# Optimization experiments

Hardware: AMD Instinct MI355X
Metric: run time of the kernel (lower is better)

## Reference

```python
import jax, jax.numpy as jnp
import numpy as np

AGENT, WIN = 6, 7

def _rel_pos_index(d, h, w):
    # same construction as the torch buffer `relative_position_index`
    coords = np.stack(np.meshgrid(np.arange(d), np.arange(h), np.arange(w), indexing='ij'))
    cf = coords.reshape(3, -1)                                   # [3, S]
    rc = (cf[:, :, None] - cf[:, None, :]).transpose(1, 2, 0).astype(np.int64)
    rc[:, :, 0] += d - 1; rc[:, :, 1] += h - 1; rc[:, :, 2] += w - 1
    rc[:, :, 0] *= (2 * h - 1) * (2 * w - 1)
    rc[:, :, 1] *= (2 * w - 1)
    return jnp.asarray(rc.sum(-1))                               # [S, S]

def setup_inputs() -> dict:
    key = jax.random.key(0)
    ks = jax.random.split(key, 11)
    b, L, X, Y, w1, w2, dim = 2, AGENT, 8, 8, WIN, WIN, 256
    heads, ch, nt = 8, 32, 2
    table = (2 * L - 1) * (2 * w1 - 1) * (2 * w2 - 1)
    f = lambda k, s: (0.02 * jax.random.normal(k, s)).astype(jnp.float32)
    return dict(
        x=jax.random.normal(ks[0], (b, L, X, Y, w1, w2, dim), jnp.float32),
        Wq=f(ks[1], (nt, dim, dim)), bq=f(ks[2], (nt, dim)),
        Wk=f(ks[3], (nt, dim, dim)), bk=f(ks[4], (nt, dim)),
        Wv=f(ks[5], (nt, dim, dim)), bv=f(ks[6], (nt, dim)),
        rel_att=f(ks[7], (nt * nt, heads, ch, ch)),
        rel_msg=f(ks[8], (nt * nt, heads, ch, ch)),
        bias_table=f(ks[9], (table, heads)),
        Wo=f(ks[10], (dim, dim)),
        agent_type=1,
    )

def reference(x, Wq, bq, Wk, bk, Wv, bv, rel_att, rel_msg, bias_table, Wo, agent_type):
    b, L, X, Y, w1, w2, dim = x.shape
    heads, ch = rel_att.shape[1], rel_att.shape[2]
    nt = Wq.shape[0]
    scale = ch ** -0.5
    # types = [0] + (agent_size-1)*[type], identical across batch (as in forward)
    types = jnp.concatenate([jnp.zeros(1, jnp.int32),
                             jnp.full((L - 1,), agent_type, jnp.int32)])

    def proj(W, bias):
        # type-indexed per-agent linear (gathered batched matmul instead of python loops)
        y = jnp.einsum('blxyuvd,lde->blxyuve', x, W[types])
        y = y + bias[types][None, :, None, None, None, None, :]
        # -> [b, n=(X*Y) windows, m heads, L agents, p=(w1*w2) tokens, c]
        return y.reshape(b, L, X * Y, w1 * w2, heads, ch).transpose(0, 2, 4, 1, 3, 5)

    q = proj(Wq, bq) * scale
    k = proj(Wk, bk)
    v = proj(Wv, bv)

    # relation weights gathered by (src_type, dst_type) pair: [m, L, L, c, c]
    rel = types[:, None] * nt + types[None, :]
    w_att = rel_att[rel].transpose(2, 0, 1, 3, 4)
    w_msg = rel_msg[rel].transpose(2, 0, 1, 3, 4)

    # bilinear hetero attention scores, grouped by agent pair (i,j)
    sim = jnp.einsum('bnmipc,mijcf,bnmjqf->bnmipjq', q, w_att, k)
    S, n = L * w1 * w2, X * Y
    sim = sim.reshape(b, n, heads, S, S)
    idx = _rel_pos_index(L, w1, w2)                                # [S, S] static
    sim = sim + bias_table[idx].transpose(2, 0, 1)                 # + [m, S, S] rel-pos bias
    attn = jax.nn.softmax(sim, axis=-1).reshape(b, n, heads, L, w1 * w2, L, w1 * w2)

    # relation-transformed messages, then attention-weighted aggregation
    vt = jnp.einsum('mijcf,bnmjqf->bnmijqc', w_msg, v)
    out = jnp.einsum('bnmipjq,bnmijqc->bnmipc', attn, vt)
    # [b, n, m, L, p, c] -> [b, L, X, Y, w1, w2, dim]
    out = out.transpose(0, 3, 1, 4, 2, 5).reshape(b, L, X, Y, w1, w2, dim)
    return out @ Wo.T
```

## Files before the change

kernel.cpp:

```cpp
#include <hip/hip_runtime.h>
#include <hip/hip_bf16.h>

typedef __hip_bfloat16 bf16;
typedef unsigned short u16;
typedef short bf16x8 __attribute__((ext_vector_type(8)));
typedef float f32x4  __attribute__((ext_vector_type(4)));

#define BB    2
#define LL    6
#define NWIN  64
#define PP    49
#define DIMM  256
#define HEADS 8
#define CHN   32
#define SS    294
#define ASTRIDE 264
#define BSTRIDE 304
#define WBSTRIDE 168

__device__ __forceinline__ u16 bfbits(float x) { return __bfloat16_as_ushort(__float2bfloat16(x)); }
__device__ __forceinline__ f32x4 mfma16(bf16x8 a, bf16x8 b, f32x4 c) {
    return __builtin_amdgcn_mfma_f32_16x16x32_bf16(a, b, c, 0, 0, 0);
}

__global__ __launch_bounds__(256) void k_prep(
    const float* __restrict__ Wq, const float* __restrict__ Wk, const float* __restrict__ Wv,
    const float* __restrict__ Wo, const float* __restrict__ ra, const float* __restrict__ rm,
    const float* __restrict__ bt,
    u16* __restrict__ wT, u16* __restrict__ Wob, u16* __restrict__ raT, u16* __restrict__ rmb,
    float* __restrict__ biasM)
{
    const int blk = blockIdx.x;
    if (blk < 1792) {
        const int idx = blk*256 + threadIdx.x;
        if (idx >= 7*65536) return;
        const int mat = idx >> 16, rem = idx & 65535;
        if (mat < 6) {
            const int tz = mat >> 1, t = mat & 1;
            const int e = rem >> 8, d = rem & 255;
            const float* W = (tz == 0 ? Wq : tz == 1 ? Wk : Wv);
            wT[mat*65536 + rem] = bfbits(W[t*65536 + d*256 + e]);
        } else {
            Wob[rem] = bfbits(Wo[rem]);
        }
    } else if (blk < 1920) {
        const int idx = (blk - 1792)*256 + threadIdx.x;
        if (idx < 4*HEADS*CHN*CHN) {
            const int pm = idx >> 10, cf = idx & 1023, c = cf >> 5, f = cf & 31;
            raT[(pm << 10) + (f << 5) + c] = bfbits(ra[idx]);
            rmb[idx] = bfbits(rm[idx]);
        }
    } else {
        const int idx = (blk - 1920)*256 + threadIdx.x;
        if (idx < HEADS*SS*BSTRIDE) {
            const int m = idx / (SS*BSTRIDE);
            const int rem = idx % (SS*BSTRIDE);
            const int s1 = rem / BSTRIDE, s2 = rem % BSTRIDE;
            float val = 0.f;
            if (s2 < SS) {
                const int i1 = s1/49, p1 = s1 - i1*49, h1 = p1/7, w1 = p1 - h1*7;
                const int j2 = s2/49, p2 = s2 - j2*49, h2 = p2/7, w2 = p2 - h2*7;
                const int rc = i1*169 + h1*13 + w1, cc = j2*169 + h2*13 + w2;
                val = bt[(rc - cc + 929)*8 + m];
            }
            biasM[idx] = val;
        }
    }
}

__global__ __launch_bounds__(256) void k_qkv2(
    const float* __restrict__ x, const u16* __restrict__ wT,
    const float* __restrict__ bq, const float* __restrict__ bk, const float* __restrict__ bv,
    const int* __restrict__ atype,
    u16* __restrict__ q, u16* __restrict__ k, u16* __restrict__ v)
{
    __shared__ __align__(16) u16 As[64*ASTRIDE];
    const int tid = threadIdx.x;
    const int w = tid >> 6, lane = tid & 63;
    const int g4 = lane >> 4, c16 = lane & 15;
    const int bid = blockIdx.x;
    const int nwin = bid & 63;
    const int l = (bid >> 6) % LL;
    const int b = bid / (LL*NWIN);

    const float4* xp = (const float4*)(x + (size_t)bid * (PP*DIMM));
    for (int idx = tid; idx < 49*64; idx += 256) {
        const int row = idx >> 6, c4 = idx & 63;
        const float4 xv = xp[idx];
        ushort4 h;
        h.x = bfbits(xv.x); h.y = bfbits(xv.y); h.z = bfbits(xv.z); h.w = bfbits(xv.w);
        *(ushort4*)&As[row*ASTRIDE + c4*4] = h;
    }
    const ushort4 z4 = {0, 0, 0, 0};
    for (int idx = tid; idx < 15*66; idx += 256) {
        const int row = 49 + idx/66, c4 = idx%66;
        *(ushort4*)&As[row*ASTRIDE + c4*4] = z4;
    }
    __syncthreads();

    const int t = (l == 0) ? 0 : atype[0];
    const f32x4 zero4 = {0.f, 0.f, 0.f, 0.f};

    for (int tz = 0; tz < 3; ++tz) {
        const u16* WT = wT + (size_t)(tz*2 + t)*65536;
        const float* bias = (tz == 0 ? bq : tz == 1 ? bk : bv) + t*DIMM;
        u16* dst = (tz == 0 ? q : tz == 1 ? k : v);
        const float scale = (tz == 0) ? 0.17677669529663687f : 1.0f;

        f32x4 acc[4][4];
        #pragma unroll
        for (int mm = 0; mm < 4; ++mm)
            #pragma unroll
            for (int nn = 0; nn < 4; ++nn) acc[mm][nn] = zero4;

        for (int ks = 0; ks < 8; ++ks) {
            bf16x8 a[4], bb[4];
            #pragma unroll
            for (int mm = 0; mm < 4; ++mm)
                a[mm] = *(const bf16x8*)&As[(mm*16 + c16)*ASTRIDE + ks*32 + g4*8];
            #pragma unroll
            for (int nn = 0; nn < 4; ++nn)
                bb[nn] = *(const bf16x8*)&WT[(size_t)(w*64 + nn*16 + c16)*256 + ks*32 + g4*8];
            #pragma unroll
            for (int mm = 0; mm < 4; ++mm)
                #pragma unroll
                for (int nn = 0; nn < 4; ++nn)
                    acc[mm][nn] = mfma16(a[mm], bb[nn], acc[mm][nn]);
        }

        #pragma unroll
        for (int nn = 0; nn < 4; ++nn) {
            const int col = w*64 + nn*16 + c16;
            const float bval = bias[col];
            const int head = col >> 5, c = col & 31;
            const size_t base = (((size_t)(b*NWIN + nwin)*HEADS + head)*SS + l*PP)*CHN + c;
            #pragma unroll
            for (int mm = 0; mm < 4; ++mm) {
                #pragma unroll
                for (int r = 0; r < 4; ++r) {
                    const int row = mm*16 + g4*4 + r;
                    if (row < PP)
                        dst[base + (size_t)row*CHN] = bfbits((acc[mm][nn][r] + bval)*scale);
                }
            }
        }
    }
}

__global__ __launch_bounds__(256) void k_attn(
    const u16* __restrict__ q, const u16* __restrict__ kk_, const u16* __restrict__ v,
    const u16* __restrict__ raT, const u16* __restrict__ rmb,
    const float* __restrict__ biasM, const int* __restrict__ atype,
    u16* __restrict__ o_pre)
{
    __shared__ __align__(16) u16 vT[32*328];
    __shared__ __align__(16) u16 vT0[32*72];
    __shared__ __align__(16) u16 wbuf[4*16*WBSTRIDE];

    const int tid  = threadIdx.x;
    const int w    = tid >> 6;
    const int lane = tid & 63;
    const int g4   = lane >> 4;
    const int c16  = lane & 15;
    const int bid  = blockIdx.x;
    const int m    = bid & 7;
    const int nwin = (bid >> 3) & 63;
    const int b    = bid >> 9;
    const int at   = atype[0];

    const size_t slab = (size_t)bid * (SS*CHN);
    const u16* qs  = q   + slab;
    const u16* ksg = kk_ + slab;
    const u16* vsg = v   + slab;
    const float* bm = biasM + (size_t)m*(SS*BSTRIDE);

    u16* wb = wbuf + w*(16*WBSTRIDE);

    for (int idx = tid; idx < 32*26; idx += 256) vT[(idx/26)*328 + 294 + (idx%26)] = 0;
    for (int idx = tid; idx < 32*15; idx += 256) vT0[(idx/15)*72 + 49 + (idx%15)] = 0;
    for (int idx = tid; idx < SS*CHN/2; idx += 256) {
        const int s2 = idx >> 4;
        const int f2 = (idx & 15) << 1;
        const unsigned int val = *(const unsigned int*)(vsg + s2*CHN + f2);
        const u16 v0 = (u16)(val & 0xffff), v1 = (u16)(val >> 16);
        vT[f2*328 + s2] = v0;
        vT[(f2+1)*328 + s2] = v1;
        if (s2 < 49) { vT0[f2*72 + s2] = v0; vT0[(f2+1)*72 + s2] = v1; }
    }
    __syncthreads();

    const f32x4 zero4 = {0.f, 0.f, 0.f, 0.f};

    for (int job = w; job < 20; job += 4) {
        const int tile = (job == 19) ? 3 : job;
        const int tiv  = (job <= 3) ? 0 : at;
        const int pair0 = tiv*2;
        const int pair1 = tiv*2 + at;

        const int rowA = tile*16 + c16;
        const bf16x8 aq = *(const bf16x8*)(qs + rowA*CHN + g4*8);
        f32x4 cqw00, cqw01, cqw10, cqw11;
        {
            const u16* base0 = raT + (pair0*HEADS + m)*1024;
            const u16* base1 = raT + (pair1*HEADS + m)*1024;
            const bf16x8 b00 = *(const bf16x8*)(base0 + (c16     )*32 + g4*8);
            const bf16x8 b01 = *(const bf16x8*)(base0 + (16 + c16)*32 + g4*8);
            const bf16x8 b10 = *(const bf16x8*)(base1 + (c16     )*32 + g4*8);
            const bf16x8 b11 = *(const bf16x8*)(base1 + (16 + c16)*32 + g4*8);
            cqw00 = mfma16(aq, b00, zero4);
            cqw01 = mfma16(aq, b01, zero4);
            cqw10 = mfma16(aq, b10, zero4);
            cqw11 = mfma16(aq, b11, zero4);
        }
        #pragma unroll
        for (int r = 0; r < 4; ++r) {
            const int row = g4*4 + r;
            wb[row*72 +      c16] = bfbits(cqw00[r]);
            wb[row*72 + 16 + c16] = bfbits(cqw01[r]);
            wb[row*72 + 32 + c16] = bfbits(cqw10[r]);
            wb[row*72 + 48 + c16] = bfbits(cqw11[r]);
        }
        const bf16x8 A0 = *(const bf16x8*)(wb + c16*72 +      g4*8);
        const bf16x8 A1 = *(const bf16x8*)(wb + c16*72 + 32 + g4*8);

        f32x4 acc[19];
        #pragma unroll
        for (int t = 0; t < 3; ++t) {
            const bf16x8 bk = *(const bf16x8*)(ksg + (t*16 + c16)*CHN + g4*8);
            acc[t] = mfma16(A0, bk, zero4);
        }
        {
            const bf16x8 bk = *(const bf16x8*)(ksg + (3*16 + c16)*CHN + g4*8);
            const f32x4 cA = mfma16(A0, bk, zero4);
            const f32x4 cB = mfma16(A1, bk, zero4);
            #pragma unroll
            for (int r = 0; r < 4; ++r) acc[3][r] = (c16 == 0) ? cA[r] : cB[r];
        }
        #pragma unroll
        for (int t = 4; t < 19; ++t) {
            const bf16x8 bk = *(const bf16x8*)(ksg + (t*16 + c16)*CHN + g4*8);
            acc[t] = mfma16(A1, bk, zero4);
        }

        const float* bmrow[4];
        #pragma unroll
        for (int r = 0; r < 4; ++r) {
            const int s1r = tile*16 + g4*4 + r;
            const int s1c = (s1r < SS) ? s1r : 293;
            bmrow[r] = bm + (size_t)s1c*BSTRIDE;
        }
        #pragma unroll
        for (int t = 0; t < 19; ++t)
            #pragma unroll
            for (int r = 0; r < 4; ++r)
                acc[t][r] += bmrow[r][t*16 + c16];
        #pragma unroll
        for (int r = 0; r < 4; ++r)
            acc[18][r] = (c16 < 6) ? acc[18][r] : -1e30f;

        float mx[4], sm[4];
        #pragma unroll
        for (int r = 0; r < 4; ++r) mx[r] = -1e30f;
        #pragma unroll
        for (int t = 0; t < 19; ++t)
            #pragma unroll
            for (int r = 0; r < 4; ++r) mx[r] = fmaxf(mx[r], acc[t][r]);
        #pragma unroll
        for (int off = 1; off < 16; off <<= 1)
            #pragma unroll
            for (int r = 0; r < 4; ++r) mx[r] = fmaxf(mx[r], __shfl_xor(mx[r], off));
        #pragma unroll
        for (int r = 0; r < 4; ++r) sm[r] = 0.f;
        #pragma unroll
        for (int t = 0; t < 19; ++t)
            #pragma unroll
            for (int r = 0; r < 4; ++r) { const float e = __expf(acc[t][r] - mx[r]); acc[t][r] = e; sm[r] += e; }
        #pragma unroll
        for (int off = 1; off < 16; off <<= 1)
            #pragma unroll
            for (int r = 0; r < 4; ++r) sm[r] += __shfl_xor(sm[r], off);
        #pragma unroll
        for (int r = 0; r < 4; ++r) {
            const float inv = 1.0f / sm[r];
            #pragma unroll
            for (int t = 0; t < 19; ++t) acc[t][r] *= inv;
        }

        f32x4 aggF0a = zero4, aggF0b = zero4, aggF1a = zero4, aggF1b = zero4;
        f32x4 agg00 = zero4, agg01 = zero4;
        bf16x8 asave0, asave1;
        #pragma unroll
        for (int t = 0; t < 10; ++t)
            #pragma unroll
            for (int r = 0; r < 4; ++r)
                wb[(g4*4 + r)*WBSTRIDE + t*16 + c16] = bfbits(acc[t][r]);
        #pragma unroll
        for (int ks = 0; ks < 5; ++ks) {
            const bf16x8 ap  = *(const bf16x8*)(wb + c16*WBSTRIDE + ks*32 + g4*8);
            const bf16x8 bv0 = *(const bf16x8*)(vT + (c16     )*328 + ks*32 + g4*8);
            const bf16x8 bv1 = *(const bf16x8*)(vT + (16 + c16)*328 + ks*32 + g4*8);
            if (ks & 1) { aggF0b = mfma16(ap, bv0, aggF0b); aggF1b = mfma16(ap, bv1, aggF1b); }
            else        { aggF0a = mfma16(ap, bv0, aggF0a); aggF1a = mfma16(ap, bv1, aggF1a); }
            if (ks == 0) asave0 = ap;
            if (ks == 1) asave1 = ap;
        }

        #pragma unroll
        for (int t2 = 0; t2 < 9; ++t2)
            #pragma unroll
            for (int r = 0; r < 4; ++r)
                wb[(g4*4 + r)*WBSTRIDE + t2*16 + c16] = bfbits(acc[10 + t2][r]);
        #pragma unroll
        for (int r = 0; r < 4; ++r)
            wb[(g4*4 + r)*WBSTRIDE + 9*16 + c16] = 0;
        #pragma unroll
        for (int ks2 = 0; ks2 < 5; ++ks2) {
            const int ks = 5 + ks2;
            const bf16x8 ap  = *(const bf16x8*)(wb + c16*WBSTRIDE + ks2*32 + g4*8);
            const bf16x8 bv0 = *(const bf16x8*)(vT + (c16     )*328 + ks*32 + g4*8);
            const bf16x8 bv1 = *(const bf16x8*)(vT + (16 + c16)*328 + ks*32 + g4*8);
            if (ks2 & 1) { aggF0b = mfma16(ap, bv0, aggF0b); aggF1b = mfma16(ap, bv1, aggF1b); }
            else         { aggF0a = mfma16(ap, bv0, aggF0a); aggF1a = mfma16(ap, bv1, aggF1a); }
        }

        {
            const bf16x8 b00 = *(const bf16x8*)(vT0 + (c16     )*72 +      g4*8);
            const bf16x8 b01 = *(const bf16x8*)(vT0 + (16 + c16)*72 +      g4*8);
            const bf16x8 b10 = *(const bf16x8*)(vT0 + (c16     )*72 + 32 + g4*8);
            const bf16x8 b11 = *(const bf16x8*)(vT0 + (16 + c16)*72 + 32 + g4*8);
            agg00 = mfma16(asave0, b00, agg00); agg00 = mfma16(asave1, b10, agg00);
            agg01 = mfma16(asave0, b01, agg01); agg01 = mfma16(asave1, b11, agg01);
        }
        const f32x4 aggF0 = aggF0a + aggF0b;
        const f32x4 aggF1 = aggF1a + aggF1b;
        const f32x4 agg10 = aggF0 - agg00;
        const f32x4 agg11 = aggF1 - agg01;

        #pragma unroll
        for (int r = 0; r < 4; ++r) {
            const int row = g4*4 + r;
            wb[row*72 +      c16] = bfbits(agg00[r]);
            wb[row*72 + 16 + c16] = bfbits(agg01[r]);
            wb[row*72 + 32 + c16] = bfbits(agg10[r]);
            wb[row*72 + 48 + c16] = bfbits(agg11[r]);
        }
        const bf16x8 aA0 = *(const bf16x8*)(wb + c16*72 +      g4*8);
        const bf16x8 aA1 = *(const bf16x8*)(wb + c16*72 + 32 + g4*8);
        const u16* mb0 = rmb + (pair0*HEADS + m)*1024;
        const u16* mb1 = rmb + (pair1*HEADS + m)*1024;
        const bf16x8 bm00 = *(const bf16x8*)(mb0 + (c16     )*32 + g4*8);
        const bf16x8 bm01 = *(const bf16x8*)(mb0 + (16 + c16)*32 + g4*8);
        const bf16x8 bm10 = *(const bf16x8*)(mb1 + (c16     )*32 + g4*8);
        const bf16x8 bm11 = *(const bf16x8*)(mb1 + (16 + c16)*32 + g4*8);
        f32x4 out0 = mfma16(aA0, bm00, zero4); out0 = mfma16(aA1, bm10, out0);
        f32x4 out1 = mfma16(aA0, bm01, zero4); out1 = mfma16(aA1, bm11, out1);

        #pragma unroll
        for (int r = 0; r < 4; ++r) {
            const int s1row = tile*16 + g4*4 + r;
            bool valid = (s1row < SS);
            if (job == 3)  valid = valid && (s1row == 48);
            if (job == 19) valid = valid && (s1row >= 49);
            if (valid) {
                const int i = s1row / 49, p = s1row - i*49;
                const size_t rb = ((size_t)((b*LL + i)*NWIN + nwin)*PP + p)*DIMM + m*CHN;
                o_pre[rb + c16]      = bfbits(out0[r]);
                o_pre[rb + 16 + c16] = bfbits(out1[r]);
            }
        }
    }
}

__global__ __launch_bounds__(256) void k_out2(
    const u16* __restrict__ pre, const u16* __restrict__ Wob,
    float* __restrict__ out)
{
    __shared__ __align__(16) u16 As[64*ASTRIDE];
    const int tid = threadIdx.x;
    const int w = tid >> 6, lane = tid & 63;
    const int g4 = lane >> 4, c16 = lane & 15;
    const int bid = blockIdx.x;

    const uint4* pp = (const uint4*)(pre + (size_t)bid * (PP*DIMM));
    for (int idx = tid; idx < 49*32; idx += 256) {
        const int row = idx >> 5, c8 = idx & 31;
        *(uint4*)&As[row*ASTRIDE + c8*8] = pp[idx];
    }
    const ushort4 z4 = {0, 0, 0, 0};
    for (int idx = tid; idx < 15*66; idx += 256) {
        const int row = 49 + idx/66, c4 = idx%66;
        *(ushort4*)&As[row*ASTRIDE + c4*4] = z4;
    }
    __syncthreads();

    const f32x4 zero4 = {0.f, 0.f, 0.f, 0.f};
    f32x4 acc[4][4];
    #pragma unroll
    for (int mm = 0; mm < 4; ++mm)
        #pragma unroll
        for (int nn = 0; nn < 4; ++nn) acc[mm][nn] = zero4;

    for (int ks = 0; ks < 8; ++ks) {
        bf16x8 a[4], bb[4];
        #pragma unroll
        for (int mm = 0; mm < 4; ++mm)
            a[mm] = *(const bf16x8*)&As[(mm*16 + c16)*ASTRIDE + ks*32 + g4*8];
        #pragma unroll
        for (int nn = 0; nn < 4; ++nn)
            bb[nn] = *(const bf16x8*)&Wob[(size_t)(w*64 + nn*16 + c16)*256 + ks*32 + g4*8];
        #pragma unroll
        for (int mm = 0; mm < 4; ++mm)
            #pragma unroll
            for (int nn = 0; nn < 4; ++nn)
                acc[mm][nn] = mfma16(a[mm], bb[nn], acc[mm][nn]);
    }

    float* op = out + (size_t)bid * (PP*DIMM);
    #pragma unroll
    for (int nn = 0; nn < 4; ++nn) {
        const int col = w*64 + nn*16 + c16;
        #pragma unroll
        for (int mm = 0; mm < 4; ++mm) {
            #pragma unroll
            for (int r = 0; r < 4; ++r) {
                const int row = mm*16 + g4*4 + r;
                if (row < PP) op[(size_t)row*DIMM + col] = acc[mm][nn][r];
            }
        }
    }
}

extern "C" void kernel_launch(void* const* d_in, const int* in_sizes, int n_in,
                              void* d_out, int out_size, void* d_ws, size_t ws_size,
                              hipStream_t stream)
{
    (void)in_sizes; (void)n_in; (void)out_size; (void)ws_size;
    const float* x        = (const float*)d_in[0];
    const float* Wq       = (const float*)d_in[1];
    const float* bq       = (const float*)d_in[2];
    const float* Wk       = (const float*)d_in[3];
    const float* bk       = (const float*)d_in[4];
    const float* Wv       = (const float*)d_in[5];
    const float* bv       = (const float*)d_in[6];
    const float* rel_att  = (const float*)d_in[7];
    const float* rel_msg  = (const float*)d_in[8];
    const float* bias_tab = (const float*)d_in[9];
    const float* Wo       = (const float*)d_in[10];
    const int*   atype    = (const int*)d_in[11];
    float* out = (float*)d_out;

    char* ws = (char*)d_ws;
    u16* wT     = (u16*)ws;
    u16* Wob    = (u16*)(ws + 786432);
    u16* raT    = (u16*)(ws + 917504);
    u16* rmb    = (u16*)(ws + 983040);
    float* biasM= (float*)(ws + 1048576);
    u16* qb     = (u16*)(ws + 3908608);
    u16* kb     = (u16*)(ws + 3908608 + 1ull*19267584);
    u16* vb     = (u16*)(ws + 3908608 + 2ull*19267584);
    u16* o_preb = (u16*)(ws + 3908608 + 3ull*19267584);

    k_prep<<<4713, 256, 0, stream>>>(Wq, Wk, Wv, Wo, rel_att, rel_msg, bias_tab,
                                     wT, Wob, raT, rmb, biasM);
    k_qkv2<<<BB*LL*NWIN, 256, 0, stream>>>(x, wT, bq, bk, bv, atype, qb, kb, vb);
    k_attn<<<BB*NWIN*HEADS, 256, 0, stream>>>(qb, kb, vb, raT, rmb, biasM, atype, o_preb);
    k_out2<<<BB*LL*NWIN, 256, 0, stream>>>(o_preb, Wob, out);
}
```

Baseline: 221.9 us.

## Split attention softmax into two online-softmax halves to cut register pressure

Instead of holding all 19 score tiles in registers, the attention kernel now computes scores, softmax and the PV product for the first 10 key tiles, then for the remaining 9, and merges the two halves with online-softmax rescaling. This roughly halves the live accumulator registers so launch_bounds(256,4) can request higher occupancy. The separate vT0 shared buffer is dropped in favour of reading from vT with a masked A operand, and LDS strides are changed. The cost is extra exponentials and rescaling arithmetic, and normalisation now happens after the bf16 probability matrix is formed, which changes rounding slightly.

```diff
diff --git a/kernel.cpp b/kernel.cpp
--- a/kernel.cpp
+++ b/kernel.cpp
@@ -16,7 +16,8 @@
 #define SS    294
 #define ASTRIDE 264
 #define BSTRIDE 304
-#define WBSTRIDE 168
+#define VSTRIDE 308
+#define PSTRIDE 164
 
 __device__ __forceinline__ u16 bfbits(float x) { return __bfloat16_as_ushort(__float2bfloat16(x)); }
 __device__ __forceinline__ f32x4 mfma16(bf16x8 a, bf16x8 b, f32x4 c) {
@@ -147,15 +148,14 @@
     }
 }
 
-__global__ __launch_bounds__(256) void k_attn(
+__global__ __launch_bounds__(256, 4) void k_attn(
     const u16* __restrict__ q, const u16* __restrict__ kk_, const u16* __restrict__ v,
     const u16* __restrict__ raT, const u16* __restrict__ rmb,
     const float* __restrict__ biasM, const int* __restrict__ atype,
     u16* __restrict__ o_pre)
 {
-    __shared__ __align__(16) u16 vT[32*328];
-    __shared__ __align__(16) u16 vT0[32*72];
-    __shared__ __align__(16) u16 wbuf[4*16*WBSTRIDE];
+    __shared__ __align__(16) u16 vT[32*VSTRIDE + 32];
+    __shared__ __align__(16) u16 wbuf[4*16*PSTRIDE];
 
     const int tid  = threadIdx.x;
     const int w    = tid >> 6;
@@ -174,22 +174,27 @@
     const u16* vsg = v   + slab;
     const float* bm = biasM + (size_t)m*(SS*BSTRIDE);
 
-    u16* wb = wbuf + w*(16*WBSTRIDE);
-
-    for (int idx = tid; idx < 32*26; idx += 256) vT[(idx/26)*328 + 294 + (idx%26)] = 0;
-    for (int idx = tid; idx < 32*15; idx += 256) vT0[(idx/15)*72 + 49 + (idx%15)] = 0;
+    u16* wb = wbuf + w*(16*PSTRIDE);
+
+    for (int idx = tid; idx < 32*(VSTRIDE - SS) + 32; idx += 256) {
+        if (idx < 32*(VSTRIDE - SS)) {
+            const int f = idx / (VSTRIDE - SS), c = idx % (VSTRIDE - SS);
+            vT[f*VSTRIDE + SS + c] = 0;
+        } else {
+            vT[32*VSTRIDE + (idx - 32*(VSTRIDE - SS))] = 0;
+        }
+    }
     for (int idx = tid; idx < SS*CHN/2; idx += 256) {
         const int s2 = idx >> 4;
         const int f2 = (idx & 15) << 1;
         const unsigned int val = *(const unsigned int*)(vsg + s2*CHN + f2);
-        const u16 v0 = (u16)(val & 0xffff), v1 = (u16)(val >> 16);
-        vT[f2*328 + s2] = v0;
-        vT[(f2+1)*328 + s2] = v1;
-        if (s2 < 49) { vT0[f2*72 + s2] = v0; vT0[(f2+1)*72 + s2] = v1; }
+        vT[f2*VSTRIDE + s2]     = (u16)(val & 0xffff);
+        vT[(f2+1)*VSTRIDE + s2] = (u16)(val >> 16);
     }
     __syncthreads();
 
     const f32x4 zero4 = {0.f, 0.f, 0.f, 0.f};
+    const bf16x8 zero8 = {0, 0, 0, 0, 0, 0, 0, 0};
 
     for (int job = w; job < 20; job += 4) {
         const int tile = (job == 19) ? 3 : job;
@@ -199,7 +204,6 @@
 
         const int rowA = tile*16 + c16;
         const bf16x8 aq = *(const bf16x8*)(qs + rowA*CHN + g4*8);
-        f32x4 cqw00, cqw01, cqw10, cqw11;
         {
             const u16* base0 = raT + (pair0*HEADS + m)*1024;
             const u16* base1 = raT + (pair1*HEADS + m)*1024;
@@ -207,40 +211,21 @@
             const bf16x8 b01 = *(const bf16x8*)(base0 + (16 + c16)*32 + g4*8);
             const bf16x8 b10 = *(const bf16x8*)(base1 + (c16     )*32 + g4*8);
             const bf16x8 b11 = *(const bf16x8*)(base1 + (16 + c16)*32 + g4*8);
-            cqw00 = mfma16(aq, b00, zero4);
-            cqw01 = mfma16(aq, b01, zero4);
-            cqw10 = mfma16(aq, b10, zero4);
-            cqw11 = mfma16(aq, b11, zero4);
-        }
-        #pragma unroll
-        for (int r = 0; r < 4; ++r) {
-            const int row = g4*4 + r;
-            wb[row*72 +      c16] = bfbits(cqw00[r]);
-            wb[row*72 + 16 + c16] = bfbits(cqw01[r]);
-            wb[row*72 + 32 + c16] = bfbits(cqw10[r]);
-            wb[row*72 + 48 + c16] = bfbits(cqw11[r]);
+            const f32x4 cqw00 = mfma16(aq, b00, zero4);
+            const f32x4 cqw01 = mfma16(aq, b01, zero4);
+            const f32x4 cqw10 = mfma16(aq, b10, zero4);
+            const f32x4 cqw11 = mfma16(aq, b11, zero4);
+            #pragma unroll
+            for (int r = 0; r < 4; ++r) {
+                const int row = g4*4 + r;
+                wb[row*72 +      c16] = bfbits(cqw00[r]);
+                wb[row*72 + 16 + c16] = bfbits(cqw01[r]);
+                wb[row*72 + 32 + c16] = bfbits(cqw10[r]);
+                wb[row*72 + 48 + c16] = bfbits(cqw11[r]);
+            }
         }
         const bf16x8 A0 = *(const bf16x8*)(wb + c16*72 +      g4*8);
         const bf16x8 A1 = *(const bf16x8*)(wb + c16*72 + 32 + g4*8);
-
-        f32x4 acc[19];
-        #pragma unroll
-        for (int t = 0; t < 3; ++t) {
-            const bf16x8 bk = *(const bf16x8*)(ksg + (t*16 + c16)*CHN + g4*8);
-            acc[t] = mfma16(A0, bk, zero4);
-        }
-        {
-            const bf16x8 bk = *(const bf16x8*)(ksg + (3*16 + c16)*CHN + g4*8);
-            const f32x4 cA = mfma16(A0, bk, zero4);
-            const f32x4 cB = mfma16(A1, bk, zero4);
-            #pragma unroll
-            for (int r = 0; r < 4; ++r) acc[3][r] = (c16 == 0) ? cA[r] : cB[r];
-        }
-        #pragma unroll
-        for (int t = 4; t < 19; ++t) {
-            const bf16x8 bk = *(const bf16x8*)(ksg + (t*16 + c16)*CHN + g4*8);
-            acc[t] = mfma16(A1, bk, zero4);
-        }
 
         const float* bmrow[4];
         #pragma unroll
@@ -249,98 +234,165 @@
             const int s1c = (s1r < SS) ? s1r : 293;
             bmrow[r] = bm + (size_t)s1c*BSTRIDE;
         }
-        #pragma unroll
-        for (int t = 0; t < 19; ++t)
-            #pragma unroll
-            for (int r = 0; r < 4; ++r)
-                acc[t][r] += bmrow[r][t*16 + c16];
-        #pragma unroll
-        for (int r = 0; r < 4; ++r)
-            acc[18][r] = (c16 < 6) ? acc[18][r] : -1e30f;
-
-        float mx[4], sm[4];
-        #pragma unroll
-        for (int r = 0; r < 4; ++r) mx[r] = -1e30f;
-        #pragma unroll
-        for (int t = 0; t < 19; ++t)
-            #pragma unroll
-            for (int r = 0; r < 4; ++r) mx[r] = fmaxf(mx[r], acc[t][r]);
-        #pragma unroll
-        for (int off = 1; off < 16; off <<= 1)
-            #pragma unroll
-            for (int r = 0; r < 4; ++r) mx[r] = fmaxf(mx[r], __shfl_xor(mx[r], off));
-        #pragma unroll
-        for (int r = 0; r < 4; ++r) sm[r] = 0.f;
-        #pragma unroll
-        for (int t = 0; t < 19; ++t)
-            #pragma unroll
-            for (int r = 0; r < 4; ++r) { const float e = __expf(acc[t][r] - mx[r]); acc[t][r] = e; sm[r] += e; }
-        #pragma unroll
-        for (int off = 1; off < 16; off <<= 1)
-            #pragma unroll
-            for (int r = 0; r < 4; ++r) sm[r] += __shfl_xor(sm[r], off);
-        #pragma unroll
-        for (int r = 0; r < 4; ++r) {
-            const float inv = 1.0f / sm[r];
-            #pragma unroll
-            for (int t = 0; t < 19; ++t) acc[t][r] *= inv;
-        }
-
-        f32x4 aggF0a = zero4, aggF0b = zero4, aggF1a = zero4, aggF1b = zero4;
-        f32x4 agg00 = zero4, agg01 = zero4;
+
+        float m1[4], s1[4];
+        f32x4 aggA0 = zero4, aggA1 = zero4, agg00 = zero4, agg01 = zero4;
+        {
+            f32x4 acc[10];
+            #pragma unroll
+            for (int t = 0; t < 3; ++t) {
+                const bf16x8 bk = *(const bf16x8*)(ksg + (t*16 + c16)*CHN + g4*8);
+                acc[t] = mfma16(A0, bk, zero4);
+            }
+            {
+                const bf16x8 bk = *(const bf16x8*)(ksg + (3*16 + c16)*CHN + g4*8);
+                const f32x4 cA = mfma16(A0, bk, zero4);
+                const f32x4 cB = mfma16(A1, bk, zero4);
+                #pragma unroll
+                for (int r = 0; r < 4; ++r) acc[3][r] = (c16 == 0) ? cA[r] : cB[r];
+            }
+            #pragma unroll
+            for (int t = 4; t < 10; ++t) {
+                const bf16x8 bk = *(const bf16x8*)(ksg + (t*16 + c16)*CHN + g4*8);
+                acc[t] = mfma16(A1, bk, zero4);
+            }
+            #pragma unroll
+            for (int t = 0; t < 10; ++t)
+                #pragma unroll
+                for (int r = 0; r < 4; ++r)
+                    acc[t][r] += bmrow[r][t*16 + c16];
+
+            #pragma unroll
+            for (int r = 0; r < 4; ++r) m1[r] = -1e30f;
+            #pragma unroll
+            for (int t = 0; t < 10; ++t)
+                #pragma unroll
+                for (int r = 0; r < 4; ++r) m1[r] = fmaxf(m1[r], acc[t][r]);
+            #pragma unroll
+            for (int off = 1; off < 16; off <<= 1)
+                #pragma unroll
+                for (int r = 0; r < 4; ++r) m1[r] = fmaxf(m1[r], __shfl_xor(m1[r], off));
+            #pragma unroll
+            for (int r = 0; r < 4; ++r) s1[r] = 0.f;
+            #pragma unroll
+            for (int t = 0; t < 10; ++t)
+                #pragma unroll
+                for (int r = 0; r < 4; ++r) { const float e = __expf(acc[t][r] - m1[r]); acc[t][r] = e; s1[r] += e; }
+            #pragma unroll
+            for (int off = 1; off < 16; off <<= 1)
+                #pragma unroll
+                for (int r = 0; r < 4; ++r) s1[r] += __shfl_xor(s1[r], off);
+
+            #pragma unroll
+            for (int t = 0; t < 10; ++t)
+                #pragma unroll
+                for (int r = 0; r < 4; ++r)
+                    wb[(g4*4 + r)*PSTRIDE + t*16 + c16] = bfbits(acc[t][r]);
+        }
+
         bf16x8 asave0, asave1;
         #pragma unroll
-        for (int t = 0; t < 10; ++t)
-            #pragma unroll
-            for (int r = 0; r < 4; ++r)
-                wb[(g4*4 + r)*WBSTRIDE + t*16 + c16] = bfbits(acc[t][r]);
-        #pragma unroll
         for (int ks = 0; ks < 5; ++ks) {
-            const bf16x8 ap  = *(const bf16x8*)(wb + c16*WBSTRIDE + ks*32 + g4*8);
-            const bf16x8 bv0 = *(const bf16x8*)(vT + (c16     )*328 + ks*32 + g4*8);
-            const bf16x8 bv1 = *(const bf16x8*)(vT + (16 + c16)*328 + ks*32 + g4*8);
-            if (ks & 1) { aggF0b = mfma16(ap, bv0, aggF0b); aggF1b = mfma16(ap, bv1, aggF1b); }
-            else        { aggF0a = mfma16(ap, bv0, aggF0a); aggF1a = mfma16(ap, bv1, aggF1a); }
+            const bf16x8 ap  = *(const bf16x8*)(wb + c16*PSTRIDE + ks*32 + g4*8);
+            const bf16x8 bv0 = *(const bf16x8*)(vT + (c16     )*VSTRIDE + ks*32 + g4*8);
+            const bf16x8 bv1 = *(const bf16x8*)(vT + (16 + c16)*VSTRIDE + ks*32 + g4*8);
+            aggA0 = mfma16(ap, bv0, aggA0);
+            aggA1 = mfma16(ap, bv1, aggA1);
             if (ks == 0) asave0 = ap;
             if (ks == 1) asave1 = ap;
         }
-
-        #pragma unroll
-        for (int t2 = 0; t2 < 9; ++t2)
+        {
+            bf16x8 a1m;
+            if (g4 < 2)       a1m = asave1;
+            else if (g4 == 2) { a1m = zero8; a1m[0] = asave1[0]; }
+            else              a1m = zero8;
+            const bf16x8 b00 = *(const bf16x8*)(vT + (c16     )*VSTRIDE +      g4*8);
+            const bf16x8 b01 = *(const bf16x8*)(vT + (16 + c16)*VSTRIDE +      g4*8);
+            const bf16x8 b10 = *(const bf16x8*)(vT + (c16     )*VSTRIDE + 32 + g4*8);
+            const bf16x8 b11 = *(const bf16x8*)(vT + (16 + c16)*VSTRIDE + 32 + g4*8);
+            agg00 = mfma16(asave0, b00, agg00); agg00 = mfma16(a1m, b10, agg00);
+            agg01 = mfma16(asave0, b01, agg01); agg01 = mfma16(a1m, b11, agg01);
+        }
+
+        float m2[4], s2v[4];
+        f32x4 aggB0 = zero4, aggB1 = zero4;
+        {
+            f32x4 acc[9];
+            #pragma unroll
+            for (int t2 = 0; t2 < 9; ++t2) {
+                const bf16x8 bk = *(const bf16x8*)(ksg + ((10 + t2)*16 + c16)*CHN + g4*8);
+                acc[t2] = mfma16(A1, bk, zero4);
+            }
+            #pragma unroll
+            for (int t2 = 0; t2 < 9; ++t2)
+                #pragma unroll
+                for (int r = 0; r < 4; ++r)
+                    acc[t2][r] += bmrow[r][(10 + t2)*16 + c16];
             #pragma unroll
             for (int r = 0; r < 4; ++r)
-                wb[(g4*4 + r)*WBSTRIDE + t2*16 + c16] = bfbits(acc[10 + t2][r]);
-        #pragma unroll
-        for (int r = 0; r < 4; ++r)
-            wb[(g4*4 + r)*WBSTRIDE + 9*16 + c16] = 0;
+                acc[8][r] = (c16 < 6) ? acc[8][r] : -1e30f;
+
+            #pragma unroll
+            for (int r = 0; r < 4; ++r) m2[r] = -1e30f;
+            #pragma unroll
+            for (int t2 = 0; t2 < 9; ++t2)
+                #pragma unroll
+                for (int r = 0; r < 4; ++r) m2[r] = fmaxf(m2[r], acc[t2][r]);
+            #pragma unroll
+            for (int off = 1; off < 16; off <<= 1)
+                #pragma unroll
+                for (int r = 0; r < 4; ++r) m2[r] = fmaxf(m2[r], __shfl_xor(m2[r], off));
+            #pragma unroll
+            for (int r = 0; r < 4; ++r) s2v[r] = 0.f;
+            #pragma unroll
+            for (int t2 = 0; t2 < 9; ++t2)
+                #pragma unroll
+                for (int r = 0; r < 4; ++r) { const float e = __expf(acc[t2][r] - m2[r]); acc[t2][r] = e; s2v[r] += e; }
+            #pragma unroll
+            for (int off = 1; off < 16; off <<= 1)
+                #pragma unroll
+                for (int r = 0; r < 4; ++r) s2v[r] += __shfl_xor(s2v[r], off);
+
+            #pragma unroll
+            for (int t2 = 0; t2 < 9; ++t2)
+                #pragma unroll
+                for (int r = 0; r < 4; ++r)
+                    wb[(g4*4 + r)*PSTRIDE + t2*16 + c16] = bfbits(acc[t2][r]);
+            #pragma unroll
+            for (int r = 0; r < 4; ++r)
+                wb[(g4*4 + r)*PSTRIDE + 9*16 + c16] = 0;
+        }
+
         #pragma unroll
         for (int ks2 = 0; ks2 < 5; ++ks2) {
-            const int ks = 5 + ks2;
-            const bf16x8 ap  = *(const bf16x8*)(wb + c16*WBSTRIDE + ks2*32 + g4*8);
-            const bf16x8 bv0 = *(const bf16x8*)(vT + (c16     )*328 + ks*32 + g4*8);
-            const bf16x8 bv1 = *(const bf16x8*)(vT + (16 + c16)*328 + ks*32 + g4*8);
-            if (ks2 & 1) { aggF0b = mfma16(ap, bv0, aggF0b); aggF1b = mfma16(ap, bv1, aggF1b); }
-            else         { aggF0a = mfma16(ap, bv0, aggF0a); aggF1a = mfma16(ap, bv1, aggF1a); }
-        }
-
-        {
-            const bf16x8 b00 = *(const bf16x8*)(vT0 + (c16     )*72 +      g4*8);
-            const bf16x8 b01 = *(const bf16x8*)(vT0 + (16 + c16)*72 +      g4*8);
-            const bf16x8 b10 = *(const bf16x8*)(vT0 + (c16     )*72 + 32 + g4*8);
-            const bf16x8 b11 = *(const bf16x8*)(vT0 + (16 + c16)*72 + 32 + g4*8);
-            agg00 = mfma16(asave0, b00, agg00); agg00 = mfma16(asave1, b10, agg00);
-            agg01 = mfma16(asave0, b01, agg01); agg01 = mfma16(asave1, b11, agg01);
-        }
-        const f32x4 aggF0 = aggF0a + aggF0b;
-        const f32x4 aggF1 = aggF1a + aggF1b;
-        const f32x4 agg10 = aggF0 - agg00;
-        const f32x4 agg11 = aggF1 - agg01;
+            const bf16x8 ap  = *(const bf16x8*)(wb + c16*PSTRIDE + ks2*32 + g4*8);
+            const bf16x8 bv0 = *(const bf16x8*)(vT + (c16     )*VSTRIDE + (5 + ks2)*32 + g4*8);
+            const bf16x8 bv1 = *(const bf16x8*)(vT + (16 + c16)*VSTRIDE + (5 + ks2)*32 + g4*8);
+            aggB0 = mfma16(ap, bv0, aggB0);
+            aggB1 = mfma16(ap, bv1, aggB1);
+        }
+
+        f32x4 aggF0, aggF1, agg0s0, agg0s1;
+        #pragma unroll
+        for (int r = 0; r < 4; ++r) {
+            const float mm2 = fmaxf(m1[r], m2[r]);
+            const float a1 = __expf(m1[r] - mm2);
+            const float a2 = __expf(m2[r] - mm2);
+            const float inv = 1.0f / (s1[r]*a1 + s2v[r]*a2);
+            const float c1 = a1*inv, c2 = a2*inv;
+            aggF0[r]  = c1*aggA0[r] + c2*aggB0[r];
+            aggF1[r]  = c1*aggA1[r] + c2*aggB1[r];
+            agg0s0[r] = c1*agg00[r];
+            agg0s1[r] = c1*agg01[r];
+        }
+        const f32x4 agg10 = aggF0 - agg0s0;
+        const f32x4 agg11 = aggF1 - agg0s1;
 
         #pragma unroll
         for (int r = 0; r < 4; ++r) {
             const int row = g4*4 + r;
-            wb[row*72 +      c16] = bfbits(agg00[r]);
-            wb[row*72 + 16 + c16] = bfbits(agg01[r]);
+            wb[row*72 +      c16] = bfbits(agg0s0[r]);
+            wb[row*72 + 16 + c16] = bfbits(agg0s1[r]);
             wb[row*72 + 32 + c16] = bfbits(agg10[r]);
             wb[row*72 + 48 + c16] = bfbits(agg11[r]);
         }
```

Measured after the change: 326.7 us. 47.3% more time.
